# Kernel tuning notes

Measured on AMD Instinct MI355X. Metric: run time of the kernel, lower is better.

The kernel has to match this reference:

```python
import jax, jax.numpy as jnp
import numpy as np

BLANK_ID = 0


def bias_norm(x, bias, log_scale):
    # icefall BiasNorm: x * exp(log_scale) / rms(x - bias), rms over channel dim
    scales = jnp.exp(log_scale) * jax.lax.rsqrt(
        jnp.mean(jnp.square(x - bias), axis=-1, keepdims=True))
    return x * scales


def setup_inputs() -> dict:
    key = jax.random.key(0)
    N, T, S = 16, 400, 5
    ENC, DEC, JOINT, V = 512, 512, 512, 2000
    OV = V - 1  # out_vocab_dim
    ks = jax.random.split(key, 16)
    f = jax.random.normal
    return {
        "encoder_out": f(ks[0], (N, T, S, ENC), jnp.float32),
        "blank_decoder_out": f(ks[1], (N, T, S, DEC), jnp.float32),
        "vocab_decoder_out": f(ks[2], (N, T, S, DEC), jnp.float32),
        # fc_encoder_proj + its BiasNorm
        "W_enc": f(ks[3], (JOINT, ENC), jnp.float32) * 0.02,
        "b_enc": jnp.zeros((JOINT,), jnp.float32),
        "bn_enc_bias": f(ks[4], (JOINT,), jnp.float32) * 0.01,
        "bn_enc_log_scale": jnp.zeros((), jnp.float32),
        # fc_blank_decoder + its BiasNorm
        "W_bdec": f(ks[5], (JOINT, DEC), jnp.float32) * 0.02,
        "b_bdec": jnp.zeros((JOINT,), jnp.float32),
        "bn_bdec_bias": f(ks[6], (JOINT,), jnp.float32) * 0.01,
        "bn_bdec_log_scale": jnp.zeros((), jnp.float32),
        # BiasNorm for vocab decoder path (over decoder_hidden_dim)
        "bn_vdec_bias": f(ks[7], (DEC,), jnp.float32) * 0.01,
        "bn_vdec_log_scale": jnp.zeros((), jnp.float32),
        # output heads
        "W_blank": f(ks[8], (1, JOINT), jnp.float32) * 0.02,
        "b_blank": jnp.zeros((1,), jnp.float32),
        "W_ev": f(ks[9], (OV, JOINT), jnp.float32) * 0.02,
        "b_ev": jnp.zeros((OV,), jnp.float32),
        "W_dv": f(ks[10], (OV, JOINT), jnp.float32) * 0.02,
        "b_dv": jnp.zeros((OV,), jnp.float32),
    }


def reference(encoder_out, blank_decoder_out, vocab_decoder_out,
              W_enc, b_enc, bn_enc_bias, bn_enc_log_scale,
              W_bdec, b_bdec, bn_bdec_bias, bn_bdec_log_scale,
              bn_vdec_bias, bn_vdec_log_scale,
              W_blank, b_blank, W_ev, b_ev, W_dv, b_dv):
    # encoder_proj: ScaledLinear -> BiasNorm
    enc = bias_norm(jnp.einsum('ntsc,jc->ntsj', encoder_out, W_enc) + b_enc,
                    bn_enc_bias, bn_enc_log_scale)
    # blank_decoder_proj: ScaledLinear -> BiasNorm
    bdec = bias_norm(jnp.einsum('ntsc,jc->ntsj', blank_decoder_out, W_bdec) + b_bdec,
                     bn_bdec_bias, bn_bdec_log_scale)
    # vocab_decoder_proj: BiasNorm -> ScaledLinear -> log_softmax
    vdec = bias_norm(vocab_decoder_out, bn_vdec_bias, bn_vdec_log_scale)
    vdec = jnp.einsum('ntsj,vj->ntsv', vdec, W_dv) + b_dv
    vocab_decoder_prob = jax.nn.log_softmax(vdec, axis=-1)
    # joint
    blank_prob = jnp.einsum('ntsj,oj->ntso', jax.nn.relu(enc + bdec), W_blank) + b_blank
    vocab_prob = jnp.einsum('ntsj,vj->ntsv', enc, W_ev) + b_ev + vocab_decoder_prob
    out = jnp.concatenate(
        [vocab_prob[..., :BLANK_ID], blank_prob, vocab_prob[..., BLANK_ID:]], axis=-1)
    return out, vocab_decoder_prob
```

## Files before the change

kernel.cpp:

```cpp
#include <hip/hip_runtime.h>


#define R_TOTAL 32000
#define OV 1999
#define WG_ROWS 2049

typedef __attribute__((ext_vector_type(8))) short bh8;
typedef __attribute__((ext_vector_type(4))) float fx4;

__device__ __forceinline__ unsigned short f2bf(float f) {
  union { float f; unsigned u; } v; v.f = f;
  unsigned r = v.u + 0x7fffu + ((v.u >> 16) & 1u);
  return (unsigned short)(r >> 16);
}
__device__ __forceinline__ float bf2f(unsigned short h) {
  union { unsigned u; float f; } v; v.u = ((unsigned)h) << 16;
  return v.f;
}
__device__ __forceinline__ void gload_lds16(const void* g, void* l) {
  __builtin_amdgcn_global_load_lds(
      (__attribute__((address_space(1))) void*)g,
      (__attribute__((address_space(3))) void*)l, 16, 0, 0);
}
__device__ __forceinline__ void st16u(float* dst, const float* src) {
  float v[4] = {src[0], src[1], src[2], src[3]};
  __builtin_memcpy((void*)dst, v, 16);
}

__global__ void wconv_kernel(const float* __restrict__ src, unsigned short* __restrict__ dst,
                             int src_rows, int dst_rows, int shift) {
  long long n = (long long)dst_rows * 512;
  for (long long i = (long long)blockIdx.x * blockDim.x + threadIdx.x; i < n;
       i += (long long)gridDim.x * blockDim.x) {
    int row = (int)(i >> 9);
    int sr = row - shift;
    dst[i] = (sr >= 0 && sr < src_rows) ? f2bf(src[(long long)sr * 512 + (i & 511)])
                                        : (unsigned short)0;
  }
}

template<int MODE>
__global__ __launch_bounds__(1024)
void proj_norm_kernel(const float* __restrict__ X,
                      const unsigned short* __restrict__ Wb,
                      const float* __restrict__ b_lin,
                      const float* __restrict__ bn_bias,
                      const float* __restrict__ log_scale,
                      unsigned short* __restrict__ enc_b,
                      const float* __restrict__ W_blank,
                      const float* __restrict__ b_blank,
                      float* __restrict__ blank)
{
  __shared__ __attribute__((aligned(16))) unsigned short As[128 * 64];
  __shared__ __attribute__((aligned(16))) unsigned short Bs[512 * 64];
  __shared__ float red[8][128];
  __shared__ float scale_s[128];

  const int tid = threadIdx.x;
  const int l  = tid & 63;
  const int lq = l >> 4;
  const int lr = l & 15;
  const int w  = tid >> 6;
  const int wr = w >> 3;
  const int wc = w & 7;
  const int rowBase = blockIdx.x * 128;

  char* AsB = (char*)As;
  char* BsB = (char*)Bs;

  fx4 acc[4][4];
#pragma unroll
  for (int m = 0; m < 4; ++m)
#pragma unroll
    for (int n = 0; n < 4; ++n)
#pragma unroll
      for (int r = 0; r < 4; ++r) acc[m][n][r] = 0.f;

  for (int kt = 0; kt < 8; ++kt) {
#pragma unroll
    for (int p = 0; p < 2; ++p) {
      int g = tid + p * 1024;
      int row = g >> 4;
      int c4  = g & 15;
      const float4 v = *(const float4*)(X + (long long)(rowBase + row) * 512 + kt * 64 + c4 * 4);
      ushort4 h;
      h.x = f2bf(v.x); h.y = f2bf(v.y); h.z = f2bf(v.z); h.w = f2bf(v.w);
      *(ushort4*)(AsB + row * 128 + ((c4 * 8) ^ ((row & 7) << 4))) = h;
    }
#pragma unroll
    for (int p = 0; p < 4; ++p) {
      int gb = (w * 4 + p) * 64;
      int g = gb + l;
      int row = g >> 3;
      int c8 = (g & 7) ^ (row & 7);
      gload_lds16(Wb + (long long)row * 512 + kt * 64 + c8 * 8, BsB + gb * 16);
    }
    __syncthreads();

#pragma unroll
    for (int kk = 0; kk < 2; ++kk) {
      const int kb = (kk * 32 + lq * 8) * 2;
      bh8 a[4];
#pragma unroll
      for (int m = 0; m < 4; ++m) {
        int row = wr * 64 + m * 16 + lr;
        a[m] = *(const bh8*)(AsB + row * 128 + (kb ^ ((row & 7) << 4)));
      }
#pragma unroll
      for (int n = 0; n < 4; ++n) {
        int brow = wc * 64 + n * 16 + lr;
        bh8 bfr = *(const bh8*)(BsB + brow * 128 + (kb ^ ((brow & 7) << 4)));
#pragma unroll
        for (int m = 0; m < 4; ++m)
          acc[m][n] = __builtin_amdgcn_mfma_f32_16x16x32_bf16(a[m], bfr, acc[m][n], 0, 0, 0);
      }
    }
    __syncthreads();
  }

  const float escale = expf(log_scale[0]);
  float bl[4], bb[4], wb[4];
#pragma unroll
  for (int n = 0; n < 4; ++n) {
    int col = wc * 64 + n * 16 + lr;
    bl[n] = b_lin[col];
    bb[n] = bn_bias[col];
    if (MODE == 1) wb[n] = W_blank[col];
  }

  float ps[4][4];
#pragma unroll
  for (int m = 0; m < 4; ++m)
#pragma unroll
    for (int r = 0; r < 4; ++r) ps[m][r] = 0.f;
#pragma unroll
  for (int m = 0; m < 4; ++m)
#pragma unroll
    for (int n = 0; n < 4; ++n)
#pragma unroll
      for (int r = 0; r < 4; ++r) {
        float v = acc[m][n][r] + bl[n];
        float d = v - bb[n];
        ps[m][r] += d * d;
      }
#pragma unroll
  for (int off = 1; off < 16; off <<= 1)
#pragma unroll
    for (int m = 0; m < 4; ++m)
#pragma unroll
      for (int r = 0; r < 4; ++r)
        ps[m][r] += __shfl_xor(ps[m][r], off);

  if (lr == 0) {
#pragma unroll
    for (int m = 0; m < 4; ++m)
#pragma unroll
      for (int r = 0; r < 4; ++r)
        red[wc][wr * 64 + m * 16 + lq * 4 + r] = ps[m][r];
  }
  __syncthreads();
  if (tid < 128) {
    float s = 0.f;
#pragma unroll
    for (int c = 0; c < 8; ++c) s += red[c][tid];
    scale_s[tid] = escale * rsqrtf(s * (1.0f / 512.0f));
  }
  __syncthreads();

  if (MODE == 0) {
#pragma unroll
    for (int m = 0; m < 4; ++m)
#pragma unroll
      for (int n = 0; n < 4; ++n)
#pragma unroll
        for (int r = 0; r < 4; ++r) {
          int rl = wr * 64 + m * 16 + lq * 4 + r;
          int col = wc * 64 + n * 16 + lr;
          float v = (acc[m][n][r] + bl[n]) * scale_s[rl];
          enc_b[(long long)(rowBase + rl) * 512 + col] = f2bf(v);
        }
  } else {
    float pb[4][4];
#pragma unroll
    for (int m = 0; m < 4; ++m)
#pragma unroll
      for (int r = 0; r < 4; ++r) pb[m][r] = 0.f;
#pragma unroll
    for (int m = 0; m < 4; ++m)
#pragma unroll
      for (int n = 0; n < 4; ++n)
#pragma unroll
        for (int r = 0; r < 4; ++r) {
          int rl = wr * 64 + m * 16 + lq * 4 + r;
          int col = wc * 64 + n * 16 + lr;
          float v = (acc[m][n][r] + bl[n]) * scale_s[rl];
          float e = bf2f(enc_b[(long long)(rowBase + rl) * 512 + col]);
          float s = e + v;
          s = s > 0.f ? s : 0.f;
          pb[m][r] += s * wb[n];
        }
#pragma unroll
    for (int off = 1; off < 16; off <<= 1)
#pragma unroll
      for (int m = 0; m < 4; ++m)
#pragma unroll
        for (int r = 0; r < 4; ++r)
          pb[m][r] += __shfl_xor(pb[m][r], off);
    if (lr == 0) {
#pragma unroll
      for (int m = 0; m < 4; ++m)
#pragma unroll
        for (int r = 0; r < 4; ++r)
          red[wc][wr * 64 + m * 16 + lq * 4 + r] = pb[m][r];
    }
    __syncthreads();
    if (tid < 128) {
      float s = 0.f;
#pragma unroll
      for (int c = 0; c < 8; ++c) s += red[c][tid];
      blank[rowBase + tid] = s + b_blank[0];
    }
  }
}

__global__ __launch_bounds__(256)
void vdec_norm_kernel(const float* __restrict__ X, const float* __restrict__ bn_bias,
                      const float* __restrict__ log_scale, unsigned short* __restrict__ dst)
{
  const int l = threadIdx.x & 63;
  const long long row = (long long)blockIdx.x * 4 + (threadIdx.x >> 6);
  const float* xr = X + row * 512 + l * 8;
  float4 v0 = *(const float4*)xr;
  float4 v1 = *(const float4*)(xr + 4);
  float xv[8] = {v0.x, v0.y, v0.z, v0.w, v1.x, v1.y, v1.z, v1.w};
  const float4 b0 = *(const float4*)(bn_bias + l * 8);
  const float4 b1 = *(const float4*)(bn_bias + l * 8 + 4);
  float bv[8] = {b0.x, b0.y, b0.z, b0.w, b1.x, b1.y, b1.z, b1.w};
  float s = 0.f;
#pragma unroll
  for (int i = 0; i < 8; ++i) { float d = xv[i] - bv[i]; s += d * d; }
#pragma unroll
  for (int off = 1; off < 64; off <<= 1) s += __shfl_xor(s, off);
  const float sc = expf(log_scale[0]) * rsqrtf(s * (1.0f / 512.0f));
  bh8 o;
#pragma unroll
  for (int i = 0; i < 8; ++i) o[i] = (short)f2bf(xv[i] * sc);
  *(bh8*)(dst + row * 512 + l * 8) = o;
}

__device__ __forceinline__ void xcd_swz_250x16(int& bx, int& by) {
  int bid = blockIdx.y * 250 + blockIdx.x;
  int swz = (bid & 7) * 500 + (bid >> 3);
  bx = swz % 250;
  by = swz / 250;
}

__global__ __launch_bounds__(256, 2)
void gemm_stats_kernel(const unsigned short* __restrict__ Abf,
                       const unsigned short* __restrict__ Wb,
                       const float* __restrict__ bias,
                       float2* __restrict__ stats)
{
  __shared__ __attribute__((aligned(16))) unsigned short As[128 * 64];
  __shared__ __attribute__((aligned(16))) unsigned short Bs[128 * 64];
  __shared__ float smax[2][128];
  __shared__ float ssum[2][128];
  const int tid = threadIdx.x;
  const int l  = tid & 63, lq = l >> 4, lr = l & 15;
  const int w  = tid >> 6;
  const int wr = w >> 1, wc = w & 1;
  int bx, by;
  xcd_swz_250x16(bx, by);
  const int rowBase = bx * 128;
  const int colBase = by * 128;
  char* AsB = (char*)As;
  char* BsB = (char*)Bs;

  fx4 acc[4][4];
#pragma unroll
  for (int m = 0; m < 4; ++m)
#pragma unroll
    for (int n = 0; n < 4; ++n)
#pragma unroll
      for (int r = 0; r < 4; ++r) acc[m][n][r] = 0.f;

  for (int kt = 0; kt < 8; ++kt) {
#pragma unroll
    for (int p = 0; p < 4; ++p) {
      int gb = (w * 4 + p) * 64;
      int g = gb + l;
      int row = g >> 3;
      int c8 = (g & 7) ^ (row & 7);
      gload_lds16(Abf + (long long)(rowBase + row) * 512 + kt * 64 + c8 * 8, AsB + gb * 16);
      gload_lds16(Wb  + (long long)(colBase + row) * 512 + kt * 64 + c8 * 8, BsB + gb * 16);
    }
    __syncthreads();
#pragma unroll
    for (int kk = 0; kk < 2; ++kk) {
      const int kb = (kk * 32 + lq * 8) * 2;
      bh8 a[4];
#pragma unroll
      for (int m = 0; m < 4; ++m) {
        int row = wr * 64 + m * 16 + lr;
        a[m] = *(const bh8*)(AsB + row * 128 + (kb ^ ((row & 7) << 4)));
      }
#pragma unroll
      for (int n = 0; n < 4; ++n) {
        int brow = wc * 64 + n * 16 + lr;
        bh8 bfr = *(const bh8*)(BsB + brow * 128 + (kb ^ ((brow & 7) << 4)));
#pragma unroll
        for (int m = 0; m < 4; ++m)
          acc[m][n] = __builtin_amdgcn_mfma_f32_16x16x32_bf16(a[m], bfr, acc[m][n], 0, 0, 0);
      }
    }
    __syncthreads();
  }

  float bl[4]; bool cv[4];
#pragma unroll
  for (int n = 0; n < 4; ++n) {
    int col = colBase + wc * 64 + n * 16 + lr;
    cv[n] = (col < OV);
    bl[n] = cv[n] ? bias[col] : 0.f;
  }

  float mloc[4][4];
#pragma unroll
  for (int m = 0; m < 4; ++m)
#pragma unroll
    for (int r = 0; r < 4; ++r) mloc[m][r] = -3.4e38f;
#pragma unroll
  for (int m = 0; m < 4; ++m)
#pragma unroll
    for (int n = 0; n < 4; ++n)
      if (cv[n])
#pragma unroll
        for (int r = 0; r < 4; ++r)
          mloc[m][r] = fmaxf(mloc[m][r], acc[m][n][r] + bl[n]);
#pragma unroll
  for (int off = 1; off < 16; off <<= 1)
#pragma unroll
    for (int m = 0; m < 4; ++m)
#pragma unroll
      for (int r = 0; r < 4; ++r)
        mloc[m][r] = fmaxf(mloc[m][r], __shfl_xor(mloc[m][r], off));
  if (lr == 0) {
#pragma unroll
    for (int m = 0; m < 4; ++m)
#pragma unroll
      for (int r = 0; r < 4; ++r)
        smax[wc][wr * 64 + m * 16 + lq * 4 + r] = mloc[m][r];
  }
  __syncthreads();
  float M[4][4];
#pragma unroll
  for (int m = 0; m < 4; ++m)
#pragma unroll
    for (int r = 0; r < 4; ++r) {
      int row = wr * 64 + m * 16 + lq * 4 + r;
      M[m][r] = fmaxf(smax[0][row], smax[1][row]);
    }
  float sl[4][4];
#pragma unroll
  for (int m = 0; m < 4; ++m)
#pragma unroll
    for (int r = 0; r < 4; ++r) sl[m][r] = 0.f;
#pragma unroll
  for (int m = 0; m < 4; ++m)
#pragma unroll
    for (int n = 0; n < 4; ++n)
      if (cv[n]) {
#pragma unroll
        for (int r = 0; r < 4; ++r) {
          float v = acc[m][n][r] + bl[n];
          sl[m][r] += __expf(v - M[m][r]);
        }
      }
#pragma unroll
  for (int off = 1; off < 16; off <<= 1)
#pragma unroll
    for (int m = 0; m < 4; ++m)
#pragma unroll
      for (int r = 0; r < 4; ++r)
        sl[m][r] += __shfl_xor(sl[m][r], off);
  if (lr == 0) {
#pragma unroll
    for (int m = 0; m < 4; ++m)
#pragma unroll
      for (int r = 0; r < 4; ++r)
        ssum[wc][wr * 64 + m * 16 + lq * 4 + r] = sl[m][r];
  }
  __syncthreads();
  if (tid < 128) {
    float2 st;
    st.x = fmaxf(smax[0][tid], smax[1][tid]);
    st.y = ssum[0][tid] + ssum[1][tid];
    stats[(long long)by * R_TOTAL + rowBase + tid] = st;
  }
}

__global__ __launch_bounds__(256)
void lz_kernel(const float2* __restrict__ stats, float* __restrict__ lz)
{
  int row = blockIdx.x * 256 + threadIdx.x;
  if (row >= R_TOTAL) return;
  float2 st[16];
  float M = -3.4e38f;
#pragma unroll
  for (int i = 0; i < 16; ++i) {
    st[i] = stats[(long long)i * R_TOTAL + row];
    M = fmaxf(M, st[i].x);
  }
  float S = 0.f;
#pragma unroll
  for (int i = 0; i < 16; ++i) S += st[i].y * __expf(st[i].x - M);
  lz[row] = M + logf(S);
}

__global__ __launch_bounds__(512, 4)
void gemm_fused_kernel(const unsigned short* __restrict__ Av_g,
                       const unsigned short* __restrict__ Ae_g,
                       const unsigned short* __restrict__ Wdv_g,
                       const unsigned short* __restrict__ Wev_g,
                       const float* __restrict__ b_dv,
                       const float* __restrict__ b_ev,
                       const float* __restrict__ lz,
                       const float* __restrict__ blank,
                       float* __restrict__ vdp,
                       float* __restrict__ outp)
{
  __shared__ __attribute__((aligned(16))) unsigned short As[128 * 64];
  __shared__ __attribute__((aligned(16))) unsigned short Bs[128 * 64];
  const int tid = threadIdx.x;
  const int l  = tid & 63, lq = l >> 4, lr = l & 15;
  const int w  = tid >> 6;
  const int wr = w >> 2;
  const int wc = w & 3;
  int bx, by;
  xcd_swz_250x16(bx, by);
  const int rowBase = bx * 128;
  const int colBase = by * 128;
  char* AsB = (char*)As;
  char* BsB = (char*)Bs;

  fx4 accV[4][2], accE[4][2];
#pragma unroll
  for (int m = 0; m < 4; ++m)
#pragma unroll
    for (int n = 0; n < 2; ++n)
#pragma unroll
      for (int r = 0; r < 4; ++r) { accV[m][n][r] = 0.f; accE[m][n][r] = 0.f; }

  for (int kt = 0; kt < 8; ++kt) {
#pragma unroll
    for (int p = 0; p < 2; ++p) {
      int gb = (w * 2 + p) * 64;
      int g = gb + l;
      int row = g >> 3;
      int c8 = (g & 7) ^ (row & 7);
      gload_lds16(Av_g  + (long long)(rowBase + row) * 512 + kt * 64 + c8 * 8, AsB + gb * 16);
      gload_lds16(Wdv_g + (long long)(colBase + row) * 512 + kt * 64 + c8 * 8, BsB + gb * 16);
    }
    __syncthreads();
#pragma unroll
    for (int kk = 0; kk < 2; ++kk) {
      const int kb = (kk * 32 + lq * 8) * 2;
      bh8 a[4];
#pragma unroll
      for (int m = 0; m < 4; ++m) {
        int row = wr * 64 + m * 16 + lr;
        a[m] = *(const bh8*)(AsB + row * 128 + (kb ^ ((row & 7) << 4)));
      }
#pragma unroll
      for (int n = 0; n < 2; ++n) {
        int brow = wc * 32 + n * 16 + lr;
        bh8 bfr = *(const bh8*)(BsB + brow * 128 + (kb ^ ((brow & 7) << 4)));
#pragma unroll
        for (int m = 0; m < 4; ++m)
          accV[m][n] = __builtin_amdgcn_mfma_f32_16x16x32_bf16(a[m], bfr, accV[m][n], 0, 0, 0);
      }
    }
    __syncthreads();
  }

  for (int kt = 0; kt < 8; ++kt) {
#pragma unroll
    for (int p = 0; p < 2; ++p) {
      int gb = (w * 2 + p) * 64;
      int g = gb + l;
      int row = g >> 3;
      int c8 = (g & 7) ^ (row & 7);
      gload_lds16(Ae_g  + (long long)(rowBase + row) * 512 + kt * 64 + c8 * 8, AsB + gb * 16);
      gload_lds16(Wev_g + (long long)(colBase + row) * 512 + kt * 64 + c8 * 8, BsB + gb * 16);
    }
    __syncthreads();
#pragma unroll
    for (int kk = 0; kk < 2; ++kk) {
      const int kb = (kk * 32 + lq * 8) * 2;
      bh8 a[4];
#pragma unroll
      for (int m = 0; m < 4; ++m) {
        int row = wr * 64 + m * 16 + lr;
        a[m] = *(const bh8*)(AsB + row * 128 + (kb ^ ((row & 7) << 4)));
      }
#pragma unroll
      for (int n = 0; n < 2; ++n) {
        int brow = wc * 32 + n * 16 + lr;
        bh8 bfr = *(const bh8*)(BsB + brow * 128 + (kb ^ ((brow & 7) << 4)));
#pragma unroll
        for (int m = 0; m < 4; ++m)
          accE[m][n] = __builtin_amdgcn_mfma_f32_16x16x32_bf16(a[m], bfr, accE[m][n], 0, 0, 0);
      }
    }
    __syncthreads();
  }

  float lzv[4][4];
#pragma unroll
  for (int m = 0; m < 4; ++m)
#pragma unroll
    for (int r = 0; r < 4; ++r)
      lzv[m][r] = lz[rowBase + wr * 64 + m * 16 + lq * 4 + r];

  float* Lvd = (float*)As;
  float* Lov = (float*)Bs;

  const int c0 = (by == 0) ? 0 : (colBase - 1);
  const int j0 = (by == 0) ? 1 : 0;
  const int Lv = min(OV, colBase + 127) - c0;

  const int flipw = (lq & 1) << 4;

#pragma unroll
  for (int c = 0; c < 4; ++c) {
    __syncthreads();
    if (wr == (c >> 1)) {
#pragma unroll
      for (int mm = 0; mm < 2; ++mm) {
        const int m = (c & 1) * 2 + mm;
#pragma unroll
        for (int n = 0; n < 2; ++n) {
          int j = wc * 32 + n * 16 + lr;
          int cg = colBase - 1 + j;
          bool v = (cg >= 0 && cg < OV);
          float bdv = v ? b_dv[cg] : 0.f;
          float bev = v ? b_ev[cg] : 0.f;
          int jx = j ^ flipw;
#pragma unroll
          for (int r = 0; r < 4; ++r) {
            int lrow = 16 * mm + lq * 4 + r;
            float vd = accV[m][n][r] + bdv - lzv[m][r];
            float ov = accE[m][n][r] + bev + vd;
            if (by == 0 && j == 0) ov = blank[rowBase + 32 * c + lrow];
            Lvd[lrow * 128 + jx] = vd;
            Lov[lrow * 128 + jx] = ov;
          }
        }
      }
    }
    __syncthreads();

#pragma unroll
    for (int pass = 0; pass < 2; ++pass) {
      int lrow = pass * 16 + (tid >> 5);
      int lane32 = tid & 31;
      int flip = ((lrow >> 2) & 1) << 4;
      long long rg = rowBase + 32 * c + lrow;
      int p = colBase + lane32 * 4;
      if (p < 2000) {
        float4 vv = *(const float4*)&Lov[lrow * 128 + ((lane32 * 4) ^ flip)];
        *(float4*)(outp + rg * 2000 + p) = vv;
      }
    }
#pragma unroll
    for (int pass = 0; pass < 2; ++pass) {
      int lrow = pass * 16 + (tid >> 5);
      int lane32 = tid & 31;
      int flip = ((lrow >> 2) & 1) << 4;
      long long rg = rowBase + 32 * c + lrow;
      int k4 = lane32 * 4;
      if (k4 < Lv) {
        float* dst = vdp + rg * OV + c0 + k4;
        int rem = Lv - k4;
        if (rem >= 4 && j0 == 0) {
          float4 vv = *(const float4*)&Lvd[lrow * 128 + (k4 ^ flip)];
          float vs[4] = {vv.x, vv.y, vv.z, vv.w};
          st16u(dst, vs);
        } else if (rem >= 4) {
          float vs[4];
#pragma unroll
          for (int q = 0; q < 4; ++q) vs[q] = Lvd[lrow * 128 + ((j0 + k4 + q) ^ flip)];
          st16u(dst, vs);
        } else {
          for (int q = 0; q < rem; ++q) dst[q] = Lvd[lrow * 128 + ((j0 + k4 + q) ^ flip)];
        }
      }
    }
  }
}

extern "C" void kernel_launch(void* const* d_in, const int* in_sizes, int n_in,
                              void* d_out, int out_size, void* d_ws, size_t ws_size,
                              hipStream_t stream) {
  const float* encoder_out  = (const float*)d_in[0];
  const float* blank_dec    = (const float*)d_in[1];
  const float* vocab_dec    = (const float*)d_in[2];
  const float* W_enc        = (const float*)d_in[3];
  const float* b_enc        = (const float*)d_in[4];
  const float* bn_enc_bias  = (const float*)d_in[5];
  const float* bn_enc_ls    = (const float*)d_in[6];
  const float* W_bdec       = (const float*)d_in[7];
  const float* b_bdec       = (const float*)d_in[8];
  const float* bn_bdec_bias = (const float*)d_in[9];
  const float* bn_bdec_ls   = (const float*)d_in[10];
  const float* bn_vdec_bias = (const float*)d_in[11];
  const float* bn_vdec_ls   = (const float*)d_in[12];
  const float* W_blank      = (const float*)d_in[13];
  const float* b_blank      = (const float*)d_in[14];
  const float* W_ev         = (const float*)d_in[15];
  const float* b_ev         = (const float*)d_in[16];
  const float* W_dv         = (const float*)d_in[17];
  const float* b_dv         = (const float*)d_in[18];

  unsigned short* Wenc_b  = (unsigned short*)d_ws;
  unsigned short* Wbdec_b = Wenc_b + 512 * 512;
  unsigned short* Wdv_g   = Wbdec_b + 512 * 512;
  unsigned short* Wev_g   = Wdv_g + (size_t)WG_ROWS * 512;
  unsigned short* enc_b   = Wev_g + (size_t)WG_ROWS * 512;
  unsigned short* vdec_b  = enc_b + (size_t)R_TOTAL * 512;
  float2* stats = (float2*)(vdec_b + (size_t)R_TOTAL * 512);
  float*  lzbuf = (float*)(stats + (size_t)R_TOTAL * 16);
  float*  blank = lzbuf + R_TOTAL;

  float* outp = (float*)d_out;
  float* vdp  = outp + (size_t)R_TOTAL * 2000;

  wconv_kernel<<<256, 256, 0, stream>>>(W_enc,  Wenc_b,  512, 512, 0);
  wconv_kernel<<<256, 256, 0, stream>>>(W_bdec, Wbdec_b, 512, 512, 0);
  wconv_kernel<<<512, 256, 0, stream>>>(W_dv,   Wdv_g,  1999, WG_ROWS, 1);
  wconv_kernel<<<512, 256, 0, stream>>>(W_ev,   Wev_g,  1999, WG_ROWS, 1);

  vdec_norm_kernel<<<8000, 256, 0, stream>>>(vocab_dec, bn_vdec_bias, bn_vdec_ls, vdec_b);
  gemm_stats_kernel<<<dim3(250, 16), 256, 0, stream>>>(vdec_b, Wdv_g + 512, b_dv, stats);
  lz_kernel<<<125, 256, 0, stream>>>(stats, lzbuf);

  proj_norm_kernel<0><<<250, 1024, 0, stream>>>(encoder_out, Wenc_b, b_enc, bn_enc_bias,
                                                bn_enc_ls, enc_b, nullptr, nullptr, nullptr);
  proj_norm_kernel<1><<<250, 1024, 0, stream>>>(blank_dec, Wbdec_b, b_bdec, bn_bdec_bias,
                                                bn_bdec_ls, enc_b, W_blank, b_blank, blank);

  gemm_fused_kernel<<<dim3(250, 16), 512, 0, stream>>>(vdec_b, enc_b, Wdv_g, Wev_g,
                                                       b_dv, b_ev, lzbuf, blank, vdp, outp);
}
```

Before: 531.8 us.

## Cache bf16 vocab-decoder logits from stats pass to skip recomputing GEMM

The stats GEMM now writes its biased logits as bf16 to a 32000x2048 workspace buffer. The fused kernel reloads these into LDS per row chunk instead of recomputing the vocab-decoder GEMM. This removes half of the fused kernel's MFMA work and its A/W loads. In exchange it adds about 131 MB of bf16 writes plus reads and extra LDS staging. It also rounds the logits to bf16 before subtracting lz, which changes precision. The path is taken only if the workspace is large enough.

```diff
diff --git a/kernel.cpp b/kernel.cpp
--- a/kernel.cpp
+++ b/kernel.cpp
@@ -255,11 +255,13 @@
   by = swz / 250;
 }
 
+template<int LOGITS>
 __global__ __launch_bounds__(256, 2)
 void gemm_stats_kernel(const unsigned short* __restrict__ Abf,
                        const unsigned short* __restrict__ Wb,
                        const float* __restrict__ bias,
-                       float2* __restrict__ stats)
+                       float2* __restrict__ stats,
+                       unsigned short* __restrict__ logits_b)
 {
   __shared__ __attribute__((aligned(16))) unsigned short As[128 * 64];
   __shared__ __attribute__((aligned(16))) unsigned short Bs[128 * 64];
@@ -397,6 +399,41 @@
     st.y = ssum[0][tid] + ssum[1][tid];
     stats[(long long)by * R_TOTAL + rowBase + tid] = st;
   }
+
+  if (LOGITS) {
+    unsigned short* Llog = As;
+#pragma unroll
+    for (int c = 0; c < 4; ++c) {
+      __syncthreads();
+      if (wr == (c >> 1)) {
+#pragma unroll
+        for (int mm = 0; mm < 2; ++mm) {
+          const int m = (c & 1) * 2 + mm;
+#pragma unroll
+          for (int n = 0; n < 4; ++n) {
+            int j = wc * 64 + n * 16 + lr;
+            int js = j ^ ((lq & 1) << 4);
+#pragma unroll
+            for (int r = 0; r < 4; ++r) {
+              int lrow = 16 * mm + lq * 4 + r;
+              Llog[lrow * 128 + js] = cv[n] ? f2bf(acc[m][n][r] + bl[n]) : (unsigned short)0;
+            }
+          }
+        }
+      }
+      __syncthreads();
+#pragma unroll
+      for (int pass = 0; pass < 2; ++pass) {
+        int slot = pass * 256 + tid;
+        int row = slot >> 4;
+        int seg = slot & 15;
+        int base = (seg * 8) ^ (((row >> 2) & 1) << 4);
+        long long rg = rowBase + 32 * c + row;
+        *(bh8*)(logits_b + rg * 2048 + colBase + seg * 8) =
+            *(const bh8*)(Llog + row * 128 + base);
+      }
+    }
+  }
 }
 
 __global__ __launch_bounds__(256)
@@ -417,11 +454,13 @@
   lz[row] = M + logf(S);
 }
 
+template<int LOGITS>
 __global__ __launch_bounds__(512, 4)
 void gemm_fused_kernel(const unsigned short* __restrict__ Av_g,
                        const unsigned short* __restrict__ Ae_g,
                        const unsigned short* __restrict__ Wdv_g,
                        const unsigned short* __restrict__ Wev_g,
+                       const unsigned short* __restrict__ logits_g,
                        const float* __restrict__ b_dv,
                        const float* __restrict__ b_ev,
                        const float* __restrict__ lz,
@@ -431,6 +470,7 @@
 {
   __shared__ __attribute__((aligned(16))) unsigned short As[128 * 64];
   __shared__ __attribute__((aligned(16))) unsigned short Bs[128 * 64];
+  __shared__ __attribute__((aligned(16))) unsigned short Llog[32 * 136];
   const int tid = threadIdx.x;
   const int l  = tid & 63, lq = l >> 4, lr = l & 15;
   const int w  = tid >> 6;
@@ -451,36 +491,38 @@
 #pragma unroll
       for (int r = 0; r < 4; ++r) { accV[m][n][r] = 0.f; accE[m][n][r] = 0.f; }
 
-  for (int kt = 0; kt < 8; ++kt) {
-#pragma unroll
-    for (int p = 0; p < 2; ++p) {
-      int gb = (w * 2 + p) * 64;
-      int g = gb + l;
-      int row = g >> 3;
-      int c8 = (g & 7) ^ (row & 7);
-      gload_lds16(Av_g  + (long long)(rowBase + row) * 512 + kt * 64 + c8 * 8, AsB + gb * 16);
-      gload_lds16(Wdv_g + (long long)(colBase + row) * 512 + kt * 64 + c8 * 8, BsB + gb * 16);
-    }
-    __syncthreads();
-#pragma unroll
-    for (int kk = 0; kk < 2; ++kk) {
-      const int kb = (kk * 32 + lq * 8) * 2;
-      bh8 a[4];
-#pragma unroll
-      for (int m = 0; m < 4; ++m) {
-        int row = wr * 64 + m * 16 + lr;
-        a[m] = *(const bh8*)(AsB + row * 128 + (kb ^ ((row & 7) << 4)));
-      }
-#pragma unroll
-      for (int n = 0; n < 2; ++n) {
-        int brow = wc * 32 + n * 16 + lr;
-        bh8 bfr = *(const bh8*)(BsB + brow * 128 + (kb ^ ((brow & 7) << 4)));
-#pragma unroll
-        for (int m = 0; m < 4; ++m)
-          accV[m][n] = __builtin_amdgcn_mfma_f32_16x16x32_bf16(a[m], bfr, accV[m][n], 0, 0, 0);
-      }
-    }
-    __syncthreads();
+  if (!LOGITS) {
+    for (int kt = 0; kt < 8; ++kt) {
+#pragma unroll
+      for (int p = 0; p < 2; ++p) {
+        int gb = (w * 2 + p) * 64;
+        int g = gb + l;
+        int row = g >> 3;
+        int c8 = (g & 7) ^ (row & 7);
+        gload_lds16(Av_g  + (long long)(rowBase + row) * 512 + kt * 64 + c8 * 8, AsB + gb * 16);
+        gload_lds16(Wdv_g + (long long)(colBase + row) * 512 + kt * 64 + c8 * 8, BsB + gb * 16);
+      }
+      __syncthreads();
+#pragma unroll
+      for (int kk = 0; kk < 2; ++kk) {
+        const int kb = (kk * 32 + lq * 8) * 2;
+        bh8 a[4];
+#pragma unroll
+        for (int m = 0; m < 4; ++m) {
+          int row = wr * 64 + m * 16 + lr;
+          a[m] = *(const bh8*)(AsB + row * 128 + (kb ^ ((row & 7) << 4)));
+        }
+#pragma unroll
+        for (int n = 0; n < 2; ++n) {
+          int brow = wc * 32 + n * 16 + lr;
+          bh8 bfr = *(const bh8*)(BsB + brow * 128 + (kb ^ ((brow & 7) << 4)));
+#pragma unroll
+          for (int m = 0; m < 4; ++m)
+            accV[m][n] = __builtin_amdgcn_mfma_f32_16x16x32_bf16(a[m], bfr, accV[m][n], 0, 0, 0);
+        }
+      }
+      __syncthreads();
+    }
   }
 
   for (int kt = 0; kt < 8; ++kt) {
@@ -528,11 +570,21 @@
   const int c0 = (by == 0) ? 0 : (colBase - 1);
   const int j0 = (by == 0) ? 1 : 0;
   const int Lv = min(OV, colBase + 127) - c0;
+  const int sc0 = (by == 0) ? 0 : (colBase - 8);
 
   const int flipw = (lq & 1) << 4;
 
 #pragma unroll
   for (int c = 0; c < 4; ++c) {
+    if (LOGITS) {
+      for (int slot = tid; slot < 544; slot += 512) {
+        int row = slot / 17;
+        int s = slot - row * 17;
+        long long rg = rowBase + 32 * c + row;
+        gload_lds16(logits_g + rg * 2048 + sc0 + s * 8,
+                    (char*)Llog + (row * 136 + s * 8) * 2);
+      }
+    }
     __syncthreads();
     if (wr == (c >> 1)) {
 #pragma unroll
@@ -546,10 +598,13 @@
           float bdv = v ? b_dv[cg] : 0.f;
           float bev = v ? b_ev[cg] : 0.f;
           int jx = j ^ flipw;
+          int lidx = (cg >= 0) ? (cg - sc0) : 0;
 #pragma unroll
           for (int r = 0; r < 4; ++r) {
             int lrow = 16 * mm + lq * 4 + r;
-            float vd = accV[m][n][r] + bdv - lzv[m][r];
+            float vd;
+            if (LOGITS) vd = bf2f(Llog[lrow * 136 + lidx]) - lzv[m][r];
+            else        vd = accV[m][n][r] + bdv - lzv[m][r];
             float ov = accE[m][n][r] + bev + vd;
             if (by == 0 && j == 0) ov = blank[rowBase + 32 * c + lrow];
             Lvd[lrow * 128 + jx] = vd;
@@ -631,6 +686,10 @@
   float2* stats = (float2*)(vdec_b + (size_t)R_TOTAL * 512);
   float*  lzbuf = (float*)(stats + (size_t)R_TOTAL * 16);
   float*  blank = lzbuf + R_TOTAL;
+  unsigned short* logits_b = (unsigned short*)(blank + R_TOTAL);
+
+  size_t need = (size_t)((char*)(logits_b + (size_t)R_TOTAL * 2048) - (char*)d_ws);
+  const bool useL = (ws_size >= need);
 
   float* outp = (float*)d_out;
   float* vdp  = outp + (size_t)R_TOTAL * 2000;
@@ -641,7 +700,12 @@
   wconv_kernel<<<512, 256, 0, stream>>>(W_ev,   Wev_g,  1999, WG_ROWS, 1);
 
   vdec_norm_kernel<<<8000, 256, 0, stream>>>(vocab_dec, bn_vdec_bias, bn_vdec_ls, vdec_b);
-  gemm_stats_kernel<<<dim3(250, 16), 256, 0, stream>>>(vdec_b, Wdv_g + 512, b_dv, stats);
+  if (useL)
+    gemm_stats_kernel<1><<<dim3(250, 16), 256, 0, stream>>>(vdec_b, Wdv_g + 512, b_dv,
+                                                            stats, logits_b);
+  else
+    gemm_stats_kernel<0><<<dim3(250, 16), 256, 0, stream>>>(vdec_b, Wdv_g + 512, b_dv,
+                                                            stats, logits_b);
   lz_kernel<<<125, 256, 0, stream>>>(stats, lzbuf);
 
   proj_norm_kernel<0><<<250, 1024, 0, stream>>>(encoder_out, Wenc_b, b_enc, bn_enc_bias,
@@ -649,6 +713,12 @@
   proj_norm_kernel<1><<<250, 1024, 0, stream>>>(blank_dec, Wbdec_b, b_bdec, bn_bdec_bias,
                                                 bn_bdec_ls, enc_b, W_blank, b_blank, blank);
 
-  gemm_fused_kernel<<<dim3(250, 16), 512, 0, stream>>>(vdec_b, enc_b, Wdv_g, Wev_g,
-                                                       b_dv, b_ev, lzbuf, blank, vdp, outp);
-}
+  if (useL)
+    gemm_fused_kernel<1><<<dim3(250, 16), 512, 0, stream>>>(vdec_b, enc_b, Wdv_g, Wev_g,
+                                                            logits_b, b_dv, b_ev, lzbuf,
+                                                            blank, vdp, outp);
+  else
+    gemm_fused_kernel<0><<<dim3(250, 16), 512, 0, stream>>>(vdec_b, enc_b, Wdv_g, Wev_g,
+                                                            logits_b, b_dv, b_ev, lzbuf,
+                                                            blank, vdp, outp);
+}
```

Measured after the change: 531.6 us. Within noise of the previous version (-0.1%).
